# Kernel tuning notes

Measured on AMD Instinct MI355X. Metric: run time of the kernel, lower is better.

The kernel has to match this reference:

```python
import jax, jax.numpy as jnp
import numpy as np

N_NODES = 50000
N_EDGES = 1600000
IN_CH, HID_CH, OUT_CH = 256, 128, 64


def setup_inputs() -> dict:
    key = jax.random.key(0)
    k1, k2, k3, k4 = jax.random.split(key, 4)
    x = jax.random.normal(k1, (N_NODES, IN_CH), dtype=jnp.float32)
    edge_index = jax.random.randint(k2, (2, N_EDGES), 0, N_NODES, dtype=jnp.int64)
    # Glorot-style init for weights, zero bias (as PyG GCNConv)
    W1 = jax.random.normal(k3, (IN_CH, HID_CH), dtype=jnp.float32) * (1.0 / np.sqrt(IN_CH))
    b1 = jnp.zeros((HID_CH,), dtype=jnp.float32)
    W2 = jax.random.normal(k4, (HID_CH, OUT_CH), dtype=jnp.float32) * (1.0 / np.sqrt(HID_CH))
    b2 = jnp.zeros((OUT_CH,), dtype=jnp.float32)
    return {"x": x, "edge_index": edge_index, "W1": W1, "b1": b1, "W2": W2, "b2": b2}


def _gcn_norm(edge_index, num_nodes):
    # PyG GCNConv default: add self-loops, symmetric normalization deg^-1/2 A deg^-1/2
    loop = jnp.arange(num_nodes, dtype=edge_index.dtype)
    src = jnp.concatenate([edge_index[0], loop])
    dst = jnp.concatenate([edge_index[1], loop])
    deg = jax.ops.segment_sum(jnp.ones_like(dst, dtype=jnp.float32), dst, num_segments=num_nodes)
    dinv = jnp.where(deg > 0, jax.lax.rsqrt(jnp.maximum(deg, 1.0)), 0.0)
    norm = dinv[src] * dinv[dst]  # [E + N]
    return src, dst, norm


def _gcn_conv(x, src, dst, norm, W, b, num_nodes):
    h = x @ W                              # [N, C_out] dense GEMM first (PyG order)
    msg = h[src] * norm[:, None]           # gather + scale, [E+N, C_out]
    out = jax.ops.segment_sum(msg, dst, num_segments=num_nodes)  # scatter-add
    return out + b


def reference(x, edge_index, W1, b1, W2, b2):
    n = x.shape[0]
    src, dst, norm = _gcn_norm(edge_index, n)
    h = _gcn_conv(x, src, dst, norm, W1, b1, n)
    h = jax.nn.relu(h)
    # F.dropout(training=self.training): eval mode -> identity
    h = _gcn_conv(h, src, dst, norm, W2, b2, n)
    return jax.nn.log_softmax(h, axis=1)
```

## Files before the change

kernel.cpp:

```cpp
#include <hip/hip_runtime.h>
#include <math.h>

#define NN 50000
#define NE 1600000
#define NBIN 391
#define BINW 128
#define STCAP 6144
#define OVFCAP 32768
#define NBLK 512
#define EPB 3125

typedef __attribute__((ext_vector_type(8))) short bf16x8;
typedef __attribute__((ext_vector_type(4))) float f32x4;
union frag_u { unsigned u[4]; bf16x8 v; };

__device__ __forceinline__ float blo(unsigned u) { return __uint_as_float(u << 16); }
__device__ __forceinline__ float bhi(unsigned u) { return __uint_as_float(u & 0xffff0000u); }
__device__ __forceinline__ unsigned bpack(float a, float b) {
    unsigned ua = __float_as_uint(a), ub = __float_as_uint(b);
    ua += 0x7fffu + ((ua >> 16) & 1u);
    ub += 0x7fffu + ((ub >> 16) & 1u);
    return (ua >> 16) | (ub & 0xffff0000u);
}
__device__ __forceinline__ unsigned short b16(float a) {
    unsigned ua = __float_as_uint(a);
    ua += 0x7fffu + ((ua >> 16) & 1u);
    return (unsigned short)(ua >> 16);
}
__device__ __forceinline__ void addrow(float* acc, uint4 v) {
    acc[0] += blo(v.x); acc[1] += bhi(v.x); acc[2] += blo(v.y); acc[3] += bhi(v.y);
    acc[4] += blo(v.z); acc[5] += bhi(v.z); acc[6] += blo(v.w); acc[7] += bhi(v.w);
}

__device__ __forceinline__ int edge_get(const void* ei, int is64, long long i) {
    return is64 ? (int)((const long long*)ei)[i] : ((const int*)ei)[i];
}

__global__ void k_detect(const unsigned int* __restrict__ e, int* flag) {
    unsigned int v = e[2 * threadIdx.x + 1];
    unsigned long long m = __ballot(v != 0u);
    if (threadIdx.x == 0) *flag = (m == 0ull) ? 1 : 0;
}

__global__ __launch_bounds__(256) void k_wcvt(const float* __restrict__ W1,
                                              const float* __restrict__ W2,
                                              unsigned short* __restrict__ Wt1,
                                              unsigned short* __restrict__ Wt2) {
    int idx = blockIdx.x * 256 + threadIdx.x;
    if (idx < 128 * 256) {
        int c = idx >> 8, k = idx & 255;
        Wt1[idx] = b16(W1[(long long)k * 128 + c]);
    }
    idx -= 128 * 256;
    if (idx >= 0 && idx < 64 * 128) {
        int c = idx >> 7, k = idx & 127;
        Wt2[idx] = b16(W2[(long long)k * 64 + c]);
    }
}

__global__ __launch_bounds__(256) void k_bin(const void* __restrict__ ei,
                                             const int* __restrict__ flag,
                                             int* __restrict__ bincnt,
                                             unsigned* __restrict__ staged,
                                             int* __restrict__ ovfcnt,
                                             unsigned* __restrict__ ovf) {
    __shared__ unsigned lpk[EPB];
    __shared__ int lhist[NBIN], lbase[NBIN], lcur[NBIN];
    int is64 = *flag;
    int t = threadIdx.x;
    long long e0 = (long long)blockIdx.x * EPB;
    for (int i = t; i < NBIN; i += 256) { lhist[i] = 0; lcur[i] = 0; }
    __syncthreads();
    for (int j = t; j < EPB; j += 256) {
        int s = edge_get(ei, is64, e0 + j);
        int d = edge_get(ei, is64, (long long)NE + e0 + j);
        unsigned p = ((unsigned)d << 16) | (unsigned)s;
        lpk[j] = p;
        atomicAdd(&lhist[d >> 7], 1);
    }
    __syncthreads();
    for (int i = t; i < NBIN; i += 256)
        lbase[i] = (lhist[i] > 0) ? atomicAdd(&bincnt[i], lhist[i]) : 0;
    __syncthreads();
    for (int j = t; j < EPB; j += 256) {
        unsigned p = lpk[j];
        int bin = p >> 23;
        int pos = lbase[bin] + atomicAdd(&lcur[bin], 1);
        if (pos < STCAP) {
            staged[(long long)bin * STCAP + pos] = p;
        } else {
            int o = atomicAdd(ovfcnt, 1);
            if (o < OVFCAP) ovf[o] = p;
        }
    }
}

__global__ __launch_bounds__(256) void k_csr(const unsigned* __restrict__ staged,
                                             const int* __restrict__ bincnt,
                                             const int* __restrict__ ovfcnt,
                                             const unsigned* __restrict__ ovf,
                                             int* __restrict__ rowstart,
                                             int* __restrict__ cnt,
                                             float* __restrict__ dinv,
                                             int* __restrict__ csr) {
    __shared__ int lcnt[BINW], lpre[BINW], lcur[BINW];
    __shared__ int red[256];
    int b = blockIdx.x, t = threadIdx.x;
    int part = 0;
    for (int i = t; i < b; i += 256) part += bincnt[i];
    red[t] = part;
    __syncthreads();
#pragma unroll
    for (int off = 128; off; off >>= 1) {
        if (t < off) red[t] += red[t + off];
        __syncthreads();
    }
    int base = red[0];
    int n = min(bincnt[b], STCAP);
    int novf = *ovfcnt;
    const unsigned* st = staged + (long long)b * STCAP;
    if (t < BINW) { lcnt[t] = 0; lcur[t] = 0; }
    __syncthreads();
    for (int j = t; j < n; j += 256) atomicAdd(&lcnt[(st[j] >> 16) & (BINW - 1)], 1);
    for (int j = t; j < novf; j += 256) {
        unsigned p = ovf[j];
        if ((int)(p >> 23) == b) atomicAdd(&lcnt[(p >> 16) & (BINW - 1)], 1);
    }
    __syncthreads();
    if (t < BINW) lpre[t] = lcnt[t];
    __syncthreads();
#pragma unroll
    for (int off = 1; off < BINW; off <<= 1) {
        int u = (t < BINW && t >= off) ? lpre[t - off] : 0;
        __syncthreads();
        if (t < BINW && t >= off) lpre[t] += u;
        __syncthreads();
    }
    if (t < BINW) {
        int c = lcnt[t];
        int ex = lpre[t] - c;
        lpre[t] = ex;
        int node = b * BINW + t;
        if (node < NN) {
            rowstart[node] = base + ex;
            cnt[node] = c;
            dinv[node] = rsqrtf((float)c + 1.0f);
        }
    }
    __syncthreads();
    for (int j = t; j < n; j += 256) {
        unsigned p = st[j];
        int dloc = (p >> 16) & (BINW - 1);
        int pos = base + lpre[dloc] + atomicAdd(&lcur[dloc], 1);
        csr[pos] = (int)(p & 0xffffu);
    }
    for (int j = t; j < novf; j += 256) {
        unsigned p = ovf[j];
        if ((int)(p >> 23) == b) {
            int dloc = (p >> 16) & (BINW - 1);
            int pos = base + lpre[dloc] + atomicAdd(&lcur[dloc], 1);
            csr[pos] = (int)(p & 0xffffu);
        }
    }
}

__global__ __launch_bounds__(256) void k_mm1(const float* __restrict__ X,
                                             const unsigned short* __restrict__ Wt,
                                             const float* __restrict__ dinv,
                                             unsigned short* __restrict__ outh) {
    int tid = threadIdx.x;
    int w = tid >> 6, l = tid & 63;
    int lr = l & 15, kg = l >> 4;
    int row = blockIdx.x * 64 + w * 16 + lr;
    long long rowc = min(row, NN - 1);
    f32x4 acc[8];
#pragma unroll
    for (int cf = 0; cf < 8; cf++) acc[cf] = {0.f, 0.f, 0.f, 0.f};
#pragma unroll
    for (int ks = 0; ks < 8; ks++) {
        int k0 = ks * 32 + kg * 8;
        const float4* p = (const float4*)(X + rowc * 256 + k0);
        float4 v0 = p[0], v1 = p[1];
        frag_u a;
        a.u[0] = bpack(v0.x, v0.y); a.u[1] = bpack(v0.z, v0.w);
        a.u[2] = bpack(v1.x, v1.y); a.u[3] = bpack(v1.z, v1.w);
#pragma unroll
        for (int cf = 0; cf < 8; cf++) {
            uint4 bb = *(const uint4*)&Wt[(cf * 16 + lr) * 256 + k0];
            frag_u b;
            b.u[0] = bb.x; b.u[1] = bb.y; b.u[2] = bb.z; b.u[3] = bb.w;
            acc[cf] = __builtin_amdgcn_mfma_f32_16x16x32_bf16(a.v, b.v, acc[cf], 0, 0, 0);
        }
    }
    int orow0 = blockIdx.x * 64 + w * 16 + kg * 4;
#pragma unroll
    for (int r = 0; r < 4; r++) {
        int orow = orow0 + r;
        if (orow < NN) {
            float s = dinv[orow];
#pragma unroll
            for (int cf = 0; cf < 8; cf++)
                outh[(long long)orow * 128 + cf * 16 + lr] = b16(s * acc[cf][r]);
        }
    }
}

__global__ __launch_bounds__(256) void k_mm2(const unsigned short* __restrict__ Xh,
                                             const unsigned short* __restrict__ Wt,
                                             const float* __restrict__ dinv,
                                             unsigned short* __restrict__ outh) {
    int tid = threadIdx.x;
    int w = tid >> 6, l = tid & 63;
    int lr = l & 15, kg = l >> 4;
    int row = blockIdx.x * 64 + w * 16 + lr;
    long long rowc = min(row, NN - 1);
    f32x4 acc[4];
#pragma unroll
    for (int cf = 0; cf < 4; cf++) acc[cf] = {0.f, 0.f, 0.f, 0.f};
#pragma unroll
    for (int ks = 0; ks < 4; ks++) {
        int k0 = ks * 32 + kg * 8;
        uint4 av = *(const uint4*)(Xh + rowc * 128 + k0);
        frag_u a;
        a.u[0] = av.x; a.u[1] = av.y; a.u[2] = av.z; a.u[3] = av.w;
#pragma unroll
        for (int cf = 0; cf < 4; cf++) {
            uint4 bb = *(const uint4*)&Wt[(cf * 16 + lr) * 128 + k0];
            frag_u b;
            b.u[0] = bb.x; b.u[1] = bb.y; b.u[2] = bb.z; b.u[3] = bb.w;
            acc[cf] = __builtin_amdgcn_mfma_f32_16x16x32_bf16(a.v, b.v, acc[cf], 0, 0, 0);
        }
    }
    int orow0 = blockIdx.x * 64 + w * 16 + kg * 4;
#pragma unroll
    for (int r = 0; r < 4; r++) {
        int orow = orow0 + r;
        if (orow < NN) {
            float s = dinv[orow];
#pragma unroll
            for (int cf = 0; cf < 4; cf++)
                outh[(long long)orow * 64 + cf * 16 + lr] = b16(s * acc[cf][r]);
        }
    }
}

__global__ __launch_bounds__(256) void k_gather_relu(const uint4* __restrict__ h,
                                                     const int* __restrict__ csr,
                                                     const int* __restrict__ rowstart,
                                                     const int* __restrict__ cnt,
                                                     const float* __restrict__ dinv,
                                                     const float* __restrict__ bias,
                                                     uint4* __restrict__ out) {
    int tid = threadIdx.x;
    int node = blockIdx.x * 16 + (tid >> 4);
    int cl = tid & 15;
    if (node >= NN) return;
    int beg = rowstart[node], n = cnt[node];
    float acc[8];
    {
        uint4 v = h[(long long)node * 16 + cl];
        acc[0] = blo(v.x); acc[1] = bhi(v.x); acc[2] = blo(v.y); acc[3] = bhi(v.y);
        acc[4] = blo(v.z); acc[5] = bhi(v.z); acc[6] = blo(v.w); acc[7] = bhi(v.w);
    }
    int j = 0;
    for (; j + 7 < n; j += 8) {
        int a0 = csr[beg + j + 0], a1 = csr[beg + j + 1];
        int a2 = csr[beg + j + 2], a3 = csr[beg + j + 3];
        int a4 = csr[beg + j + 4], a5 = csr[beg + j + 5];
        int a6 = csr[beg + j + 6], a7 = csr[beg + j + 7];
        uint4 v0 = h[(long long)a0 * 16 + cl], v1 = h[(long long)a1 * 16 + cl];
        uint4 v2 = h[(long long)a2 * 16 + cl], v3 = h[(long long)a3 * 16 + cl];
        uint4 v4 = h[(long long)a4 * 16 + cl], v5 = h[(long long)a5 * 16 + cl];
        uint4 v6 = h[(long long)a6 * 16 + cl], v7 = h[(long long)a7 * 16 + cl];
        addrow(acc, v0); addrow(acc, v1); addrow(acc, v2); addrow(acc, v3);
        addrow(acc, v4); addrow(acc, v5); addrow(acc, v6); addrow(acc, v7);
    }
    for (; j + 3 < n; j += 4) {
        int a0 = csr[beg + j + 0], a1 = csr[beg + j + 1];
        int a2 = csr[beg + j + 2], a3 = csr[beg + j + 3];
        uint4 v0 = h[(long long)a0 * 16 + cl], v1 = h[(long long)a1 * 16 + cl];
        uint4 v2 = h[(long long)a2 * 16 + cl], v3 = h[(long long)a3 * 16 + cl];
        addrow(acc, v0); addrow(acc, v1); addrow(acc, v2); addrow(acc, v3);
    }
    for (; j < n; j++) addrow(acc, h[(long long)csr[beg + j] * 16 + cl]);
    float d = dinv[node];
    float4 b0 = *(const float4*)&bias[cl * 8];
    float4 b1 = *(const float4*)&bias[cl * 8 + 4];
    float r0 = fmaxf(fmaf(d, acc[0], b0.x), 0.f), r1 = fmaxf(fmaf(d, acc[1], b0.y), 0.f);
    float r2 = fmaxf(fmaf(d, acc[2], b0.z), 0.f), r3 = fmaxf(fmaf(d, acc[3], b0.w), 0.f);
    float r4 = fmaxf(fmaf(d, acc[4], b1.x), 0.f), r5 = fmaxf(fmaf(d, acc[5], b1.y), 0.f);
    float r6 = fmaxf(fmaf(d, acc[6], b1.z), 0.f), r7 = fmaxf(fmaf(d, acc[7], b1.w), 0.f);
    uint4 o;
    o.x = bpack(r0, r1); o.y = bpack(r2, r3); o.z = bpack(r4, r5); o.w = bpack(r6, r7);
    out[(long long)node * 16 + cl] = o;
}

__global__ __launch_bounds__(256) void k_gather_lsm(const uint4* __restrict__ h,
                                                    const int* __restrict__ csr,
                                                    const int* __restrict__ rowstart,
                                                    const int* __restrict__ cnt,
                                                    const float* __restrict__ dinv,
                                                    const float* __restrict__ bias,
                                                    float* __restrict__ out) {
    int tid = threadIdx.x;
    int node = blockIdx.x * 32 + (tid >> 3);
    int cl = tid & 7;
    if (node >= NN) return;
    int beg = rowstart[node], n = cnt[node];
    float acc[8];
    {
        uint4 v = h[(long long)node * 8 + cl];
        acc[0] = blo(v.x); acc[1] = bhi(v.x); acc[2] = blo(v.y); acc[3] = bhi(v.y);
        acc[4] = blo(v.z); acc[5] = bhi(v.z); acc[6] = blo(v.w); acc[7] = bhi(v.w);
    }
    int j = 0;
    for (; j + 7 < n; j += 8) {
        int a0 = csr[beg + j + 0], a1 = csr[beg + j + 1];
        int a2 = csr[beg + j + 2], a3 = csr[beg + j + 3];
        int a4 = csr[beg + j + 4], a5 = csr[beg + j + 5];
        int a6 = csr[beg + j + 6], a7 = csr[beg + j + 7];
        uint4 v0 = h[(long long)a0 * 8 + cl], v1 = h[(long long)a1 * 8 + cl];
        uint4 v2 = h[(long long)a2 * 8 + cl], v3 = h[(long long)a3 * 8 + cl];
        uint4 v4 = h[(long long)a4 * 8 + cl], v5 = h[(long long)a5 * 8 + cl];
        uint4 v6 = h[(long long)a6 * 8 + cl], v7 = h[(long long)a7 * 8 + cl];
        addrow(acc, v0); addrow(acc, v1); addrow(acc, v2); addrow(acc, v3);
        addrow(acc, v4); addrow(acc, v5); addrow(acc, v6); addrow(acc, v7);
    }
    for (; j + 3 < n; j += 4) {
        int a0 = csr[beg + j + 0], a1 = csr[beg + j + 1];
        int a2 = csr[beg + j + 2], a3 = csr[beg + j + 3];
        uint4 v0 = h[(long long)a0 * 8 + cl], v1 = h[(long long)a1 * 8 + cl];
        uint4 v2 = h[(long long)a2 * 8 + cl], v3 = h[(long long)a3 * 8 + cl];
        addrow(acc, v0); addrow(acc, v1); addrow(acc, v2); addrow(acc, v3);
    }
    for (; j < n; j++) addrow(acc, h[(long long)csr[beg + j] * 8 + cl]);
    float d = dinv[node];
    float4 b0 = *(const float4*)&bias[cl * 8];
    float4 b1 = *(const float4*)&bias[cl * 8 + 4];
    float t[8];
    t[0] = fmaf(d, acc[0], b0.x); t[1] = fmaf(d, acc[1], b0.y);
    t[2] = fmaf(d, acc[2], b0.z); t[3] = fmaf(d, acc[3], b0.w);
    t[4] = fmaf(d, acc[4], b1.x); t[5] = fmaf(d, acc[5], b1.y);
    t[6] = fmaf(d, acc[6], b1.z); t[7] = fmaf(d, acc[7], b1.w);
    float m = t[0];
#pragma unroll
    for (int i = 1; i < 8; i++) m = fmaxf(m, t[i]);
#pragma unroll
    for (int o = 1; o < 8; o <<= 1) m = fmaxf(m, __shfl_xor(m, o));
    float ex = 0.f;
#pragma unroll
    for (int i = 0; i < 8; i++) ex += __expf(t[i] - m);
#pragma unroll
    for (int o = 1; o < 8; o <<= 1) ex += __shfl_xor(ex, o);
    float l = logf(ex);
    float4 w0 = {t[0] - m - l, t[1] - m - l, t[2] - m - l, t[3] - m - l};
    float4 w1 = {t[4] - m - l, t[5] - m - l, t[6] - m - l, t[7] - m - l};
    *(float4*)&out[(long long)node * 64 + cl * 8] = w0;
    *(float4*)&out[(long long)node * 64 + cl * 8 + 4] = w1;
}

extern "C" void kernel_launch(void* const* d_in, const int* in_sizes, int n_in,
                              void* d_out, int out_size, void* d_ws, size_t ws_size,
                              hipStream_t stream) {
    const float* x  = (const float*)d_in[0];
    const void*  ei = d_in[1];
    const float* W1 = (const float*)d_in[2];
    const float* b1 = (const float*)d_in[3];
    const float* W2 = (const float*)d_in[4];
    const float* b2 = (const float*)d_in[5];
    float* out = (float*)d_out;

    char* ws = (char*)d_ws;
    float*          dinv     = (float*)   (ws + 0x000000);
    int*            flag     = (int*)     (ws + 0x040000);
    int*            cnt      = (int*)     (ws + 0x050000);
    int*            rowstart = (int*)     (ws + 0x090000);
    int*            bincnt   = (int*)     (ws + 0x0D0000);
    int*            ovfcnt   = (int*)     (ws + 0x0D0000 + NBIN * 4);
    unsigned*       ovf      = (unsigned*)(ws + 0x0E0000);
    int*            csr      = (int*)     (ws + 0x120000);
    unsigned short* Wt1      = (unsigned short*)(ws + 0x740000);
    unsigned short* Wt2      = (unsigned short*)(ws + 0x750000);
    unsigned short* h1       = (unsigned short*)(ws + 0x760000);
    unsigned short* out1     = (unsigned short*)(ws + 0x1400000);
    unsigned*       staged   = (unsigned*)(ws + 0x1400000);

    k_detect<<<1, 64, 0, stream>>>((const unsigned int*)ei, flag);
    k_wcvt<<<(128 * 256 + 64 * 128 + 255) / 256, 256, 0, stream>>>(W1, W2, Wt1, Wt2);
    hipMemsetAsync(bincnt, 0, (size_t)(NBIN + 1) * 4, stream);
    k_bin<<<NBLK, 256, 0, stream>>>(ei, flag, bincnt, staged, ovfcnt, ovf);
    k_csr<<<NBIN, 256, 0, stream>>>(staged, bincnt, ovfcnt, ovf, rowstart, cnt, dinv, csr);

    k_mm1<<<(NN + 63) / 64, 256, 0, stream>>>(x, Wt1, dinv, h1);
    k_gather_relu<<<(NN + 15) / 16, 256, 0, stream>>>((const uint4*)h1, csr, rowstart, cnt,
                                                      dinv, b1, (uint4*)out1);

    k_mm2<<<(NN + 63) / 64, 256, 0, stream>>>(out1, Wt2, dinv, h1);
    k_gather_lsm<<<(NN + 31) / 32, 256, 0, stream>>>((const uint4*)h1, csr, rowstart, cnt,
                                                     dinv, b2, out);
}
```

Before: 262.7 us.

## Split feature matrices into 32-channel slabs and gather each slab separately

Intermediate feature matrices now use a column-slab layout: blocks of 32 bf16 channels, each stored contiguously across all nodes. The first-layer gather runs as four launches, one per slab, so each pass touches a 3.2 MB working set that can stay resident in cache. The mm2 and second-layer gather are updated to read and write the slab layout, and the 8-wide unrolled inner loops are removed. The cost is more kernel launches and re-reading the CSR indices four times, with only 64-byte rows fetched per neighbor.

```diff
diff --git a/kernel.cpp b/kernel.cpp
--- a/kernel.cpp
+++ b/kernel.cpp
@@ -200,7 +200,8 @@
             float s = dinv[orow];
 #pragma unroll
             for (int cf = 0; cf < 8; cf++)
-                outh[(long long)orow * 128 + cf * 16 + lr] = b16(s * acc[cf][r]);
+                outh[(size_t)(cf >> 1) * NN * 32 + (long long)orow * 32 + (cf & 1) * 16 + lr] =
+                    b16(s * acc[cf][r]);
         }
     }
 }
@@ -220,7 +221,7 @@
 #pragma unroll
     for (int ks = 0; ks < 4; ks++) {
         int k0 = ks * 32 + kg * 8;
-        uint4 av = *(const uint4*)(Xh + rowc * 128 + k0);
+        uint4 av = *(const uint4*)(Xh + (size_t)ks * NN * 32 + rowc * 32 + kg * 8);
         frag_u a;
         a.u[0] = av.x; a.u[1] = av.y; a.u[2] = av.z; a.u[3] = av.w;
 #pragma unroll
@@ -239,63 +240,52 @@
             float s = dinv[orow];
 #pragma unroll
             for (int cf = 0; cf < 4; cf++)
-                outh[(long long)orow * 64 + cf * 16 + lr] = b16(s * acc[cf][r]);
-        }
-    }
-}
-
-__global__ __launch_bounds__(256) void k_gather_relu(const uint4* __restrict__ h,
-                                                     const int* __restrict__ csr,
-                                                     const int* __restrict__ rowstart,
-                                                     const int* __restrict__ cnt,
-                                                     const float* __restrict__ dinv,
-                                                     const float* __restrict__ bias,
-                                                     uint4* __restrict__ out) {
+                outh[(size_t)(cf >> 1) * NN * 32 + (long long)orow * 32 + (cf & 1) * 16 + lr] =
+                    b16(s * acc[cf][r]);
+        }
+    }
+}
+
+__global__ __launch_bounds__(256) void k_gather_relu_s(const uint4* __restrict__ h,
+                                                       const int* __restrict__ csr,
+                                                       const int* __restrict__ rowstart,
+                                                       const int* __restrict__ cnt,
+                                                       const float* __restrict__ dinv,
+                                                       const float* __restrict__ bias,
+                                                       uint4* __restrict__ out) {
     int tid = threadIdx.x;
-    int node = blockIdx.x * 16 + (tid >> 4);
-    int cl = tid & 15;
+    int node = blockIdx.x * 64 + (tid >> 2);
+    int ln = tid & 3;
     if (node >= NN) return;
     int beg = rowstart[node], n = cnt[node];
     float acc[8];
     {
-        uint4 v = h[(long long)node * 16 + cl];
+        uint4 v = h[(long long)node * 4 + ln];
         acc[0] = blo(v.x); acc[1] = bhi(v.x); acc[2] = blo(v.y); acc[3] = bhi(v.y);
         acc[4] = blo(v.z); acc[5] = bhi(v.z); acc[6] = blo(v.w); acc[7] = bhi(v.w);
     }
     int j = 0;
-    for (; j + 7 < n; j += 8) {
-        int a0 = csr[beg + j + 0], a1 = csr[beg + j + 1];
-        int a2 = csr[beg + j + 2], a3 = csr[beg + j + 3];
-        int a4 = csr[beg + j + 4], a5 = csr[beg + j + 5];
-        int a6 = csr[beg + j + 6], a7 = csr[beg + j + 7];
-        uint4 v0 = h[(long long)a0 * 16 + cl], v1 = h[(long long)a1 * 16 + cl];
-        uint4 v2 = h[(long long)a2 * 16 + cl], v3 = h[(long long)a3 * 16 + cl];
-        uint4 v4 = h[(long long)a4 * 16 + cl], v5 = h[(long long)a5 * 16 + cl];
-        uint4 v6 = h[(long long)a6 * 16 + cl], v7 = h[(long long)a7 * 16 + cl];
-        addrow(acc, v0); addrow(acc, v1); addrow(acc, v2); addrow(acc, v3);
-        addrow(acc, v4); addrow(acc, v5); addrow(acc, v6); addrow(acc, v7);
-    }
     for (; j + 3 < n; j += 4) {
         int a0 = csr[beg + j + 0], a1 = csr[beg + j + 1];
         int a2 = csr[beg + j + 2], a3 = csr[beg + j + 3];
-        uint4 v0 = h[(long long)a0 * 16 + cl], v1 = h[(long long)a1 * 16 + cl];
-        uint4 v2 = h[(long long)a2 * 16 + cl], v3 = h[(long long)a3 * 16 + cl];
+        uint4 v0 = h[(long long)a0 * 4 + ln], v1 = h[(long long)a1 * 4 + ln];
+        uint4 v2 = h[(long long)a2 * 4 + ln], v3 = h[(long long)a3 * 4 + ln];
         addrow(acc, v0); addrow(acc, v1); addrow(acc, v2); addrow(acc, v3);
     }
-    for (; j < n; j++) addrow(acc, h[(long long)csr[beg + j] * 16 + cl]);
+    for (; j < n; j++) addrow(acc, h[(long long)csr[beg + j] * 4 + ln]);
     float d = dinv[node];
-    float4 b0 = *(const float4*)&bias[cl * 8];
-    float4 b1 = *(const float4*)&bias[cl * 8 + 4];
+    float4 b0 = *(const float4*)&bias[ln * 8];
+    float4 b1 = *(const float4*)&bias[ln * 8 + 4];
     float r0 = fmaxf(fmaf(d, acc[0], b0.x), 0.f), r1 = fmaxf(fmaf(d, acc[1], b0.y), 0.f);
     float r2 = fmaxf(fmaf(d, acc[2], b0.z), 0.f), r3 = fmaxf(fmaf(d, acc[3], b0.w), 0.f);
     float r4 = fmaxf(fmaf(d, acc[4], b1.x), 0.f), r5 = fmaxf(fmaf(d, acc[5], b1.y), 0.f);
     float r6 = fmaxf(fmaf(d, acc[6], b1.z), 0.f), r7 = fmaxf(fmaf(d, acc[7], b1.w), 0.f);
     uint4 o;
     o.x = bpack(r0, r1); o.y = bpack(r2, r3); o.z = bpack(r4, r5); o.w = bpack(r6, r7);
-    out[(long long)node * 16 + cl] = o;
-}
-
-__global__ __launch_bounds__(256) void k_gather_lsm(const uint4* __restrict__ h,
+    out[(long long)node * 4 + ln] = o;
+}
+
+__global__ __launch_bounds__(256) void k_gather_lsm(const unsigned short* __restrict__ h2,
                                                     const int* __restrict__ csr,
                                                     const int* __restrict__ rowstart,
                                                     const int* __restrict__ cnt,
@@ -306,34 +296,23 @@
     int node = blockIdx.x * 32 + (tid >> 3);
     int cl = tid & 7;
     if (node >= NN) return;
+    const uint4* h = (const uint4*)(h2 + (size_t)(cl >> 2) * NN * 32) + (cl & 3);
     int beg = rowstart[node], n = cnt[node];
     float acc[8];
     {
-        uint4 v = h[(long long)node * 8 + cl];
+        uint4 v = h[(long long)node * 4];
         acc[0] = blo(v.x); acc[1] = bhi(v.x); acc[2] = blo(v.y); acc[3] = bhi(v.y);
         acc[4] = blo(v.z); acc[5] = bhi(v.z); acc[6] = blo(v.w); acc[7] = bhi(v.w);
     }
     int j = 0;
-    for (; j + 7 < n; j += 8) {
-        int a0 = csr[beg + j + 0], a1 = csr[beg + j + 1];
-        int a2 = csr[beg + j + 2], a3 = csr[beg + j + 3];
-        int a4 = csr[beg + j + 4], a5 = csr[beg + j + 5];
-        int a6 = csr[beg + j + 6], a7 = csr[beg + j + 7];
-        uint4 v0 = h[(long long)a0 * 8 + cl], v1 = h[(long long)a1 * 8 + cl];
-        uint4 v2 = h[(long long)a2 * 8 + cl], v3 = h[(long long)a3 * 8 + cl];
-        uint4 v4 = h[(long long)a4 * 8 + cl], v5 = h[(long long)a5 * 8 + cl];
-        uint4 v6 = h[(long long)a6 * 8 + cl], v7 = h[(long long)a7 * 8 + cl];
-        addrow(acc, v0); addrow(acc, v1); addrow(acc, v2); addrow(acc, v3);
-        addrow(acc, v4); addrow(acc, v5); addrow(acc, v6); addrow(acc, v7);
-    }
     for (; j + 3 < n; j += 4) {
         int a0 = csr[beg + j + 0], a1 = csr[beg + j + 1];
         int a2 = csr[beg + j + 2], a3 = csr[beg + j + 3];
-        uint4 v0 = h[(long long)a0 * 8 + cl], v1 = h[(long long)a1 * 8 + cl];
-        uint4 v2 = h[(long long)a2 * 8 + cl], v3 = h[(long long)a3 * 8 + cl];
+        uint4 v0 = h[(long long)a0 * 4], v1 = h[(long long)a1 * 4];
+        uint4 v2 = h[(long long)a2 * 4], v3 = h[(long long)a3 * 4];
         addrow(acc, v0); addrow(acc, v1); addrow(acc, v2); addrow(acc, v3);
     }
-    for (; j < n; j++) addrow(acc, h[(long long)csr[beg + j] * 8 + cl]);
+    for (; j < n; j++) addrow(acc, h[(long long)csr[beg + j] * 4]);
     float d = dinv[node];
     float4 b0 = *(const float4*)&bias[cl * 8];
     float4 b1 = *(const float4*)&bias[cl * 8 + 4];
@@ -392,10 +371,11 @@
     k_csr<<<NBIN, 256, 0, stream>>>(staged, bincnt, ovfcnt, ovf, rowstart, cnt, dinv, csr);
 
     k_mm1<<<(NN + 63) / 64, 256, 0, stream>>>(x, Wt1, dinv, h1);
-    k_gather_relu<<<(NN + 15) / 16, 256, 0, stream>>>((const uint4*)h1, csr, rowstart, cnt,
-                                                      dinv, b1, (uint4*)out1);
+    for (int s = 0; s < 4; s++)
+        k_gather_relu_s<<<(NN + 63) / 64, 256, 0, stream>>>(
+            (const uint4*)(h1 + (size_t)s * NN * 32), csr, rowstart, cnt, dinv,
+            b1 + s * 32, (uint4*)(out1 + (size_t)s * NN * 32));
 
     k_mm2<<<(NN + 63) / 64, 256, 0, stream>>>(out1, Wt2, dinv, h1);
-    k_gather_lsm<<<(NN + 31) / 32, 256, 0, stream>>>((const uint4*)h1, csr, rowstart, cnt,
-                                                     dinv, b2, out);
-}
+    k_gather_lsm<<<(NN + 31) / 32, 256, 0, stream>>>(h1, csr, rowstart, cnt, dinv, b2, out);
+}
```

New measurement: 296.6 us. 12.9% more time.
